# Performance work log

Measured on AMD Instinct MI355X. Metric: run time of the kernel, lower is better.

Reference implementation:

```python
import jax, jax.numpy as jnp
import numpy as np

N_ANCHORS = 9
OUTPUT_STRIDE = 16
TOP_N = 2000
NMS_IOU_THRESH = 0.7
MIN_SIZE = 0.01
EPS = 1e-7  # K.epsilon()


def setup_inputs() -> dict:
    key = jax.random.key(0)
    k1, k2 = jax.random.split(key)
    b, h, w = 8, 64, 64  # 1024px image / stride 16
    scores = jax.random.uniform(k1, (b, h, w, N_ANCHORS), jnp.float32)
    offsets = jax.random.normal(k2, (b, h, w, 4 * N_ANCHORS), jnp.float32) * 0.2
    scales = np.array([128.0, 256.0, 512.0])
    ratios = np.array([0.5, 1.0, 2.0])
    aw = (scales[:, None] * np.sqrt(ratios)[None, :]).reshape(-1)
    ah = (scales[:, None] / np.sqrt(ratios)[None, :]).reshape(-1)
    anchors = jnp.asarray(np.stack([aw, ah], axis=-1), jnp.float32)  # [9,2]
    return {"scores": scores, "offsets": offsets, "anchors": anchors}


def _pairwise_iou(a, b):
    # a: [N,4], b: [M,4] (x1,y1,x2,y2) -> [N,M]
    a = a[:, None, :]
    b = b[None, :, :]
    mins = jnp.maximum(a[..., :2], b[..., :2])
    maxs = jnp.minimum(a[..., 2:], b[..., 2:])
    wh = jnp.maximum(maxs - mins, 0.0)
    inter = wh[..., 0] * wh[..., 1]
    area_a = (a[..., 2] - a[..., 0]) * (a[..., 3] - a[..., 1])
    area_b = (b[..., 2] - b[..., 0]) * (b[..., 3] - b[..., 1])
    return inter / (area_a + area_b - inter + EPS)


def _nms_pad(boxes):
    # boxes: [N,4] already sorted by descending score (output of top_k).
    # Greedy NMS (matches tf.image.non_max_suppression semantics), keep order,
    # zero-pad suppressed tail (matches tf.pad to top_n in the original).
    N = boxes.shape[0]
    iou = _pairwise_iou(boxes, boxes)  # [N,N]
    idx = jnp.arange(N)

    def body(i, keep):
        suppress = keep[i] & (iou[i] > NMS_IOU_THRESH) & (idx > i)
        return keep & ~suppress

    keep = jax.lax.fori_loop(0, N, body, jnp.ones((N,), bool))
    sort_keys = jnp.where(keep, idx, N)          # kept indices first, in score order
    order = jnp.argsort(sort_keys)
    valid = (jnp.sort(sort_keys) < N).astype(boxes.dtype)
    return boxes[order] * valid[:, None]


def reference(scores, offsets, anchors):
    b, h, w, K = scores.shape
    off = offsets.reshape(b, h, w, K, 4)
    # anchor decode
    gx, gy = jnp.meshgrid(jnp.arange(w), jnp.arange(h))          # [h,w] each
    center = (jnp.stack([gx, gy], -1).astype(jnp.float32) + 0.5) * OUTPUT_STRIDE  # [h,w,2]
    center = center[:, :, None, :]                               # [h,w,1,2]
    img_wh = jnp.array([w, h], jnp.float32) * OUTPUT_STRIDE
    anc = anchors.reshape(1, 1, 1, K, 2)
    pred_wh = jnp.exp(off[..., 2:]) * anc / img_wh               # [b,h,w,K,2]
    pred_xcyc = (anc * off[..., :2] + center) / img_wh
    box5 = jnp.concatenate([pred_xcyc - pred_wh / 2.0,
                            pred_xcyc + pred_wh / 2.0,
                            scores[..., None]], axis=-1)         # [b,h,w,K,5]
    # filter: clip to [0,1], zero out tiny boxes
    box5 = jnp.clip(box5, 0.0, 1.0)
    wh = box5[..., 2:4] - box5[..., 0:2]
    valid = ((wh[..., 0] > MIN_SIZE) & (wh[..., 1] > MIN_SIZE)).astype(box5.dtype)
    box5 = box5 * valid[..., None]
    box5 = box5.reshape(b, -1, 5)                                # [b, h*w*K, 5]
    # per-image top-k by score, then NMS, then zero-pad to TOP_N
    _, top_i = jax.lax.top_k(box5[..., 4], TOP_N)                # [b, TOP_N]
    top_boxes = jnp.take_along_axis(box5[..., :4], top_i[..., None], axis=1)
    proposals = jax.vmap(_nms_pad)(top_boxes)                    # [b, TOP_N, 4]
    return proposals
```

## Files before the change

### kernel.cpp

```cpp
#include <hip/hip_runtime.h>
#include <stdint.h>

#pragma clang fp contract(off)

#define BATCH 8
#define HH 64
#define WW 64
#define KA 9
#define NBOX (HH * WW * KA)
#define TOPN 2000
#define NPAD 2048
#define NW 32
#define IOU_T 0.7f
#define MINSZ 0.01f
#define EPSF 1e-7f
#define TSTRIDE 33
#define CANDCAP 3072

typedef unsigned int u32;
typedef unsigned long long u64;

__device__ __forceinline__ float clamp01(float x) { return fminf(fmaxf(x, 0.0f), 1.0f); }

__device__ __forceinline__ void bar_lds()
{
    asm volatile("s_waitcnt lgkmcnt(0)" ::: "memory");
    __builtin_amdgcn_s_barrier();
}

__device__ __forceinline__ void decode_one(
    const float* __restrict__ scores, const float4* __restrict__ offsets,
    const float* __restrict__ anchors, int gid, int t,
    float4* boxOut, u32* keyOut)
{
    int k = t % KA;
    int pos = t / KA;
    int wx = pos & (WW - 1);
    int hy = pos >> 6;
    float s = scores[gid];
    float4 off = offsets[gid];
    float aw = anchors[2 * k], ah = anchors[2 * k + 1];
    float cx = ((float)wx + 0.5f) * 16.0f;
    float cy = ((float)hy + 0.5f) * 16.0f;
    float pw = (expf(off.z) * aw) / 1024.0f;
    float ph = (expf(off.w) * ah) / 1024.0f;
    float xc = (aw * off.x + cx) / 1024.0f;
    float yc = (ah * off.y + cy) / 1024.0f;
    float x1 = clamp01(xc - pw * 0.5f);
    float y1 = clamp01(yc - ph * 0.5f);
    float x2 = clamp01(xc + pw * 0.5f);
    float y2 = clamp01(yc + ph * 0.5f);
    float sc = clamp01(s);
    float m = ((x2 - x1) > MINSZ && (y2 - y1) > MINSZ) ? 1.0f : 0.0f;
    *boxOut = make_float4(x1 * m, y1 * m, x2 * m, y2 * m);
    *keyOut = __float_as_uint(sc * m);
}

__global__ __launch_bounds__(256) void decode_kernel(
    const float* __restrict__ scores, const float4* __restrict__ offsets,
    const float* __restrict__ anchors, u32* __restrict__ keys)
{
    int gid = blockIdx.x * 256 + threadIdx.x;
    int b = gid / NBOX;
    int t = gid - b * NBOX;
    float4 box; u32 key;
    decode_one(scores, offsets, anchors, gid, t, &box, &key);
    keys[gid] = key;
}

__global__ __launch_bounds__(1024) void select_kernel(
    const u32* __restrict__ keys, const float* __restrict__ scores,
    const float4* __restrict__ offsets, const float* __restrict__ anchors,
    float4* __restrict__ topBoxes)
{
    int b = blockIdx.x;
    int tid = threadIdx.x;
    const u32* kb = keys + (size_t)b * NBOX;

    __shared__ u32 hist[4096];
    __shared__ u32 suf[1024];
    __shared__ u64 sel[NPAD];
    __shared__ u64 cand[CANDCAP];
    __shared__ u32 Bsh;
    __shared__ int Rsh;
    __shared__ int ctr, cctr;

    for (int i = tid; i < 4096; i += 1024) hist[i] = 0;
    if (tid == 0) { ctr = 0; cctr = 0; }
    __syncthreads();
    for (int i = tid; i < NBOX; i += 1024)
        atomicAdd(&hist[kb[i] >> 20], 1u);
    __syncthreads();

    int r = TOPN;
    {
        u32 s = hist[4 * tid] + hist[4 * tid + 1] + hist[4 * tid + 2] + hist[4 * tid + 3];
        suf[tid] = s;
        __syncthreads();
        for (int d = 1; d < 1024; d <<= 1) {
            u32 v = (tid + d < 1024) ? suf[tid + d] : 0u;
            __syncthreads();
            suf[tid] += v;
            __syncthreads();
        }
        u32 mine = suf[tid];
        u32 nxt = (tid < 1023) ? suf[tid + 1] : 0u;
        if (mine >= (u32)r && nxt < (u32)r) {
            u32 cum = nxt;
            for (int v = 4 * tid + 3; v >= 4 * tid; --v) {
                u32 hv = hist[v];
                cum += hv;
                if (cum >= (u32)r) { Bsh = (u32)v; Rsh = r - (int)(cum - hv); break; }
            }
        }
        __syncthreads();
    }
    u32 P1 = Bsh;
    int r1 = Rsh;
    __syncthreads();

    for (int i = tid; i < NPAD; i += 1024) sel[i] = 0ull;
    __syncthreads();
    int lane = tid & 63;
    for (int i = tid; i < NBOX; i += 1024) {
        u32 key = kb[i];
        u32 top = key >> 20;
        u64 K = ((u64)key << 16) | (u64)(0xFFFFu - (u32)i);
        bool def = (top > P1);
        bool cnd = (top == P1);
        u64 bd = __ballot(def);
        u64 bc = __ballot(cnd);
        int based = 0, basec = 0;
        if (lane == 0) {
            if (bd) based = atomicAdd(&ctr, (int)__popcll(bd));
            if (bc) basec = atomicAdd(&cctr, (int)__popcll(bc));
        }
        based = __shfl(based, 0);
        basec = __shfl(basec, 0);
        if (def) {
            int slot = based + (int)__popcll(bd & ((1ull << lane) - 1ull));
            if (slot < NPAD) sel[slot] = K;
        }
        if (cnd) {
            int cslot = basec + (int)__popcll(bc & ((1ull << lane) - 1ull));
            if (cslot < CANDCAP) cand[cslot] = K;
        }
    }
    __syncthreads();
    int cc = cctr < CANDCAP ? cctr : CANDCAP;

    u64 prefix = (u64)P1;
    r = r1;
    for (int p = 0; p < 3; ++p) {
        int shift = 24 - 12 * p;
        for (int i = tid; i < 4096; i += 1024) hist[i] = 0;
        __syncthreads();
        for (int c = tid; c < cc; c += 1024) {
            u64 K = cand[c];
            if ((K >> (shift + 12)) == prefix)
                atomicAdd(&hist[(u32)((K >> shift) & 0xFFFull)], 1u);
        }
        __syncthreads();
        u32 s = hist[4 * tid] + hist[4 * tid + 1] + hist[4 * tid + 2] + hist[4 * tid + 3];
        suf[tid] = s;
        __syncthreads();
        for (int d = 1; d < 1024; d <<= 1) {
            u32 v = (tid + d < 1024) ? suf[tid + d] : 0u;
            __syncthreads();
            suf[tid] += v;
            __syncthreads();
        }
        u32 mine = suf[tid];
        u32 nxt = (tid < 1023) ? suf[tid + 1] : 0u;
        if (mine >= (u32)r && nxt < (u32)r) {
            u32 cum = nxt;
            for (int v = 4 * tid + 3; v >= 4 * tid; --v) {
                u32 hv = hist[v];
                cum += hv;
                if (cum >= (u32)r) { Bsh = (u32)v; Rsh = r - (int)(cum - hv); break; }
            }
        }
        __syncthreads();
        prefix = (prefix << 12) | (u64)Bsh;
        r = Rsh;
        __syncthreads();
    }
    u64 T48 = prefix;

    for (int c = tid; c < cc; c += 1024) {
        u64 K = cand[c];
        bool take = (K >= T48);
        u64 bal = __ballot(take);
        int base = 0;
        if (lane == 0 && bal) base = atomicAdd(&ctr, (int)__popcll(bal));
        base = __shfl(base, 0);
        if (take) {
            int slot = base + (int)__popcll(bal & ((1ull << lane) - 1ull));
            if (slot < NPAD) sel[slot] = K;
        }
    }
    __syncthreads();

    for (int k = 2; k <= NPAD; k <<= 1) {
        for (int j = k >> 1; j > 0; j >>= 1) {
#pragma unroll
            for (int n = 0; n < 2; ++n) {
                int i = tid + n * 1024;
                int ixj = i ^ j;
                if (ixj > i) {
                    bool desc = ((i & k) == 0);
                    u64 a = sel[i], c = sel[ixj];
                    if (desc ? (a < c) : (a > c)) { sel[i] = c; sel[ixj] = a; }
                }
            }
            __syncthreads();
        }
    }

    for (int i = tid; i < NPAD; i += 1024) {
        float4 v = make_float4(0, 0, 0, 0);
        if (i < TOPN) {
            u64 K = sel[i];
            int idx = 0xFFFF - (int)(K & 0xFFFFull);
            u32 kdummy;
            decode_one(scores, offsets, anchors, b * NBOX + idx, idx, &v, &kdummy);
        }
        topBoxes[b * NPAD + i] = v;
    }
}

__global__ __launch_bounds__(256) void iou_kernel(
    const float4* __restrict__ topBoxes, u64* __restrict__ sup)
{
    int gid = blockIdx.x * 256 + threadIdx.x;
    int wid = gid >> 6;
    int lane = gid & 63;
    int b = wid / TOPN;
    int r = wid - b * TOPN;

    float4 A = topBoxes[(size_t)b * NPAD + r];
    float areaA = (A.z - A.x) * (A.w - A.y);
    size_t supBase = ((size_t)b * NPAD + r) * NW;

    for (int w = r >> 6; w < NW; ++w) {
        int j = w * 64 + lane;
        float4 Bx = topBoxes[(size_t)b * NPAD + j];
        float ix1 = fmaxf(A.x, Bx.x);
        float iy1 = fmaxf(A.y, Bx.y);
        float ix2 = fminf(A.z, Bx.z);
        float iy2 = fminf(A.w, Bx.w);
        float iw = fmaxf(ix2 - ix1, 0.0f);
        float ih = fmaxf(iy2 - iy1, 0.0f);
        float inter = iw * ih;
        float areaB = (Bx.z - Bx.x) * (Bx.w - Bx.y);
        float iou = inter / (areaA + areaB - inter + EPSF);
        bool s = (iou > IOU_T) && (j > r) && (j < TOPN);
        u64 m = __ballot(s);
        if (lane == 0) sup[supBase + w] = m;
    }
}

__global__ __launch_bounds__(256) void resolve_kernel(
    const u64* __restrict__ sup, const float4* __restrict__ topBoxes,
    float4* __restrict__ out)
{
    int b = blockIdx.x;
    int tid = threadIdx.x;
    __shared__ u64 tile[2][64 * TSTRIDE];
    __shared__ u64 keep[NW];
    __shared__ u64 nzmap[NW];
    __shared__ int wbase[NW];
    if (tid < NW) keep[tid] = (tid < 31) ? ~0ull : 0xFFFFull;
    const u64* supB = sup + (size_t)b * NPAD * NW;
    unsigned* keep32 = (unsigned*)keep;

    int row = tid >> 2;
    int wcol = (tid & 3) * 8;

    {
        const uint4* src = (const uint4*)(supB + tid * 8);
        uint4 p0 = src[0], p1 = src[1], p2 = src[2], p3 = src[3];
        u64* d = &tile[0][row * TSTRIDE + wcol];
        d[0] = ((u64)p0.y << 32) | p0.x;  d[1] = ((u64)p0.w << 32) | p0.z;
        d[2] = ((u64)p1.y << 32) | p1.x;  d[3] = ((u64)p1.w << 32) | p1.z;
        d[4] = ((u64)p2.y << 32) | p2.x;  d[5] = ((u64)p2.w << 32) | p2.z;
        d[6] = ((u64)p3.y << 32) | p3.x;  d[7] = ((u64)p3.w << 32) | p3.z;
    }
    bar_lds();

    for (int w = 0; w < NW; ++w) {
        int buf = w & 1;
        uint4 n0, n1, n2, n3;
        if (w + 1 < NW) {
            const uint4* src = (const uint4*)(supB + (size_t)(w + 1) * 2048 + tid * 8);
            n0 = src[0]; n1 = src[1]; n2 = src[2]; n3 = src[3];
        }

        if (tid < 64) {
            u64 m = tile[buf][tid * TSTRIDE + w];
            u64 later = 0;
            for (int w2 = w + 1; w2 < NW; ++w2) later |= tile[buf][tid * TSTRIDE + w2];
            u64 nzAny = __ballot((m | later) != 0ull);
            u64 nzDiag = __ballot(m != 0ull);
            u32 mlo = (u32)m, mhi = (u32)(m >> 32);
            u64 kw64 = keep[w];
            u32 kwlo = (u32)__builtin_amdgcn_readfirstlane((int)(u32)kw64);
            u32 kwhi = (u32)__builtin_amdgcn_readfirstlane((int)(u32)(kw64 >> 32));
            u64 kw = ((u64)kwhi << 32) | kwlo;
            u64 rem = kw & nzDiag;
            while (rem) {
                int t2 = (int)(__ffsll((unsigned long long)rem) - 1);
                u32 alo = (u32)__builtin_amdgcn_readlane((int)mlo, t2);
                u32 ahi = (u32)__builtin_amdgcn_readlane((int)mhi, t2);
                u64 mt = ((u64)ahi << 32) | alo;
                kw &= ~mt;
                rem &= ~(mt | (1ull << t2));
            }
            if (tid == 0) { keep[w] = kw; nzmap[w] = nzAny; }
        }
        bar_lds();

        u64 gate = keep[w] & nzmap[w];
        int w2 = tid & 31;
        int grp = tid >> 5;
        if (w2 > w && gate) {
            u64 acc = 0;
#pragma unroll
            for (int q = 0; q < 8; ++q) {
                int rl = grp * 8 + q;
                if ((gate >> rl) & 1ull)
                    acc |= tile[buf][rl * TSTRIDE + w2];
            }
            if (acc) {
                u32 lo = (u32)acc, hi = (u32)(acc >> 32);
                if (lo) atomicAnd(&keep32[2 * w2], ~lo);
                if (hi) atomicAnd(&keep32[2 * w2 + 1], ~hi);
            }
        }

        if (w + 1 < NW) {
            u64* d = &tile[buf ^ 1][row * TSTRIDE + wcol];
            d[0] = ((u64)n0.y << 32) | n0.x;  d[1] = ((u64)n0.w << 32) | n0.z;
            d[2] = ((u64)n1.y << 32) | n1.x;  d[3] = ((u64)n1.w << 32) | n1.z;
            d[4] = ((u64)n2.y << 32) | n2.x;  d[5] = ((u64)n2.w << 32) | n2.z;
            d[6] = ((u64)n3.y << 32) | n3.x;  d[7] = ((u64)n3.w << 32) | n3.z;
        }
        bar_lds();
    }

    if (tid == 0) {
        int s = 0;
        for (int w2 = 0; w2 < NW; ++w2) { wbase[w2] = s; s += __popcll(keep[w2]); }
    }
    __syncthreads();
    for (int i = tid; i < TOPN; i += 256)
        out[(size_t)b * TOPN + i] = make_float4(0, 0, 0, 0);
    __syncthreads();
    for (int i = tid; i < TOPN; i += 256) {
        int wi = i >> 6, bz = i & 63;
        u64 kw = keep[wi];
        if ((kw >> bz) & 1ull) {
            int pos = wbase[wi] + __popcll(kw & ((1ull << bz) - 1ull));
            out[(size_t)b * TOPN + pos] = topBoxes[(size_t)b * NPAD + i];
        }
    }
}

extern "C" void kernel_launch(void* const* d_in, const int* in_sizes, int n_in,
                              void* d_out, int out_size, void* d_ws, size_t ws_size,
                              hipStream_t stream)
{
    const float*  scores  = (const float*)d_in[0];
    const float4* offsets = (const float4*)d_in[1];
    const float*  anchors = (const float*)d_in[2];
    float4* out = (float4*)d_out;

    char* ws = (char*)d_ws;
    u64*    sup      = (u64*)(ws);
    u32*    keys     = (u32*)(ws + 4194304);
    float4* topBoxes = (float4*)(ws + 5373952);

    decode_kernel<<<(BATCH * NBOX) / 256, 256, 0, stream>>>(scores, offsets, anchors, keys);
    select_kernel<<<BATCH, 1024, 0, stream>>>(keys, scores, offsets, anchors, topBoxes);
    iou_kernel<<<(BATCH * TOPN * 64) / 256, 256, 0, stream>>>(topBoxes, sup);
    resolve_kernel<<<BATCH, 256, 0, stream>>>(sup, topBoxes, out);
}
```

Baseline: 124.4 us.

## Build top-bits histogram in decode kernel and speed up select radix passes

Moves the first-level 12-bit key histogram out of the single-block-per-image select kernel into the massively parallel decode kernel using global atomics, with a new zero kernel to clear it. Replaces the barrier-heavy 1024-thread LDS suffix scan with a two-level single-wavefront shuffle scan for rank finding. The compaction loop now reads keys as uint4 and batches the per-wave atomic reservations over four keys. This trades an extra launch and contended global atomics for much less serial work inside the 8-block select kernel.

```diff
diff --git a/kernel.cpp b/kernel.cpp
--- a/kernel.cpp
+++ b/kernel.cpp
@@ -56,9 +56,16 @@
     *keyOut = __float_as_uint(sc * m);
 }
 
+__global__ __launch_bounds__(256) void zero_kernel(uint4* __restrict__ p, int n)
+{
+    int g = blockIdx.x * 256 + threadIdx.x;
+    if (g < n) p[g] = make_uint4(0, 0, 0, 0);
+}
+
 __global__ __launch_bounds__(256) void decode_kernel(
     const float* __restrict__ scores, const float4* __restrict__ offsets,
-    const float* __restrict__ anchors, u32* __restrict__ keys)
+    const float* __restrict__ anchors, u32* __restrict__ keys,
+    u32* __restrict__ ghist)
 {
     int gid = blockIdx.x * 256 + threadIdx.x;
     int b = gid / NBOX;
@@ -66,91 +73,126 @@
     float4 box; u32 key;
     decode_one(scores, offsets, anchors, gid, t, &box, &key);
     keys[gid] = key;
+    atomicAdd(&ghist[(b << 12) + (key >> 20)], 1u);
+}
+
+__device__ __forceinline__ void rank_find_4096(
+    const u32* __restrict__ histL, u32* __restrict__ partial,
+    int r, u32* Bsh, int* Rsh, int tid)
+{
+    partial[tid] = histL[4 * tid] + histL[4 * tid + 1]
+                 + histL[4 * tid + 2] + histL[4 * tid + 3];
+    __syncthreads();
+    if (tid < 64) {
+        int lane = tid;
+        u32 s = 0;
+#pragma unroll
+        for (int q = 0; q < 16; ++q) s += partial[lane * 16 + q];
+        u32 suf = s;
+#pragma unroll
+        for (int d = 1; d < 64; d <<= 1) {
+            u32 t = __shfl_down(suf, d);
+            if (lane + d < 64) suf += t;
+        }
+        u32 nxt = __shfl_down(suf, 1);
+        if (lane == 63) nxt = 0;
+        bool cross = (suf >= (u32)r) && (nxt < (u32)r);
+        u64 bal = __ballot(cross);
+        int L = (int)(__ffsll((unsigned long long)bal) - 1);
+        u32 above = __shfl(nxt, L);
+        u32 hv = histL[64 * L + lane];
+        u32 suf2 = hv;
+#pragma unroll
+        for (int d = 1; d < 64; d <<= 1) {
+            u32 t = __shfl_down(suf2, d);
+            if (lane + d < 64) suf2 += t;
+        }
+        u32 nxt2 = __shfl_down(suf2, 1);
+        if (lane == 63) nxt2 = 0;
+        u32 mine2 = suf2 + above;
+        nxt2 += above;
+        if (mine2 >= (u32)r && nxt2 < (u32)r) {
+            *Bsh = (u32)(64 * L + lane);
+            *Rsh = r - (int)nxt2;
+        }
+    }
+    __syncthreads();
 }
 
 __global__ __launch_bounds__(1024) void select_kernel(
-    const u32* __restrict__ keys, const float* __restrict__ scores,
-    const float4* __restrict__ offsets, const float* __restrict__ anchors,
-    float4* __restrict__ topBoxes)
+    const u32* __restrict__ keys, const u32* __restrict__ ghist,
+    const float* __restrict__ scores, const float4* __restrict__ offsets,
+    const float* __restrict__ anchors, float4* __restrict__ topBoxes)
 {
     int b = blockIdx.x;
     int tid = threadIdx.x;
+    int lane = tid & 63;
     const u32* kb = keys + (size_t)b * NBOX;
 
     __shared__ u32 hist[4096];
-    __shared__ u32 suf[1024];
+    __shared__ u32 partial[1024];
     __shared__ u64 sel[NPAD];
     __shared__ u64 cand[CANDCAP];
     __shared__ u32 Bsh;
     __shared__ int Rsh;
     __shared__ int ctr, cctr;
 
-    for (int i = tid; i < 4096; i += 1024) hist[i] = 0;
     if (tid == 0) { ctr = 0; cctr = 0; }
-    __syncthreads();
-    for (int i = tid; i < NBOX; i += 1024)
-        atomicAdd(&hist[kb[i] >> 20], 1u);
-    __syncthreads();
-
-    int r = TOPN;
-    {
-        u32 s = hist[4 * tid] + hist[4 * tid + 1] + hist[4 * tid + 2] + hist[4 * tid + 3];
-        suf[tid] = s;
-        __syncthreads();
-        for (int d = 1; d < 1024; d <<= 1) {
-            u32 v = (tid + d < 1024) ? suf[tid + d] : 0u;
-            __syncthreads();
-            suf[tid] += v;
-            __syncthreads();
-        }
-        u32 mine = suf[tid];
-        u32 nxt = (tid < 1023) ? suf[tid + 1] : 0u;
-        if (mine >= (u32)r && nxt < (u32)r) {
-            u32 cum = nxt;
-            for (int v = 4 * tid + 3; v >= 4 * tid; --v) {
-                u32 hv = hist[v];
-                cum += hv;
-                if (cum >= (u32)r) { Bsh = (u32)v; Rsh = r - (int)(cum - hv); break; }
-            }
-        }
-        __syncthreads();
-    }
+    for (int i = tid; i < 4096; i += 1024) hist[i] = ghist[(b << 12) + i];
+    for (int i = tid; i < NPAD; i += 1024) sel[i] = 0ull;
+    __syncthreads();
+    rank_find_4096(hist, partial, TOPN, &Bsh, &Rsh, tid);
     u32 P1 = Bsh;
     int r1 = Rsh;
     __syncthreads();
 
-    for (int i = tid; i < NPAD; i += 1024) sel[i] = 0ull;
-    __syncthreads();
-    int lane = tid & 63;
-    for (int i = tid; i < NBOX; i += 1024) {
-        u32 key = kb[i];
-        u32 top = key >> 20;
-        u64 K = ((u64)key << 16) | (u64)(0xFFFFu - (u32)i);
-        bool def = (top > P1);
-        bool cnd = (top == P1);
-        u64 bd = __ballot(def);
-        u64 bc = __ballot(cnd);
+    const uint4* kb4 = (const uint4*)kb;
+#pragma unroll 1
+    for (int it = 0; it < NBOX / 4096; ++it) {
+        int i4 = it * 1024 + tid;
+        uint4 kv = kb4[i4];
+        u32 karr[4] = { kv.x, kv.y, kv.z, kv.w };
+        u64 bd[4], bc[4];
+        int totd = 0, totc = 0;
+#pragma unroll
+        for (int q = 0; q < 4; ++q) {
+            u32 top = karr[q] >> 20;
+            bd[q] = __ballot(top > P1);
+            bc[q] = __ballot(top == P1);
+            totd += (int)__popcll(bd[q]);
+            totc += (int)__popcll(bc[q]);
+        }
         int based = 0, basec = 0;
         if (lane == 0) {
-            if (bd) based = atomicAdd(&ctr, (int)__popcll(bd));
-            if (bc) basec = atomicAdd(&cctr, (int)__popcll(bc));
+            if (totd) based = atomicAdd(&ctr, totd);
+            if (totc) basec = atomicAdd(&cctr, totc);
         }
         based = __shfl(based, 0);
         basec = __shfl(basec, 0);
-        if (def) {
-            int slot = based + (int)__popcll(bd & ((1ull << lane) - 1ull));
-            if (slot < NPAD) sel[slot] = K;
-        }
-        if (cnd) {
-            int cslot = basec + (int)__popcll(bc & ((1ull << lane) - 1ull));
-            if (cslot < CANDCAP) cand[cslot] = K;
+        u64 lmask = (1ull << lane) - 1ull;
+        int offd = 0, offc = 0;
+#pragma unroll
+        for (int q = 0; q < 4; ++q) {
+            u32 key = karr[q];
+            int i = i4 * 4 + q;
+            u64 K = ((u64)key << 16) | (u64)(0xFFFFu - (u32)i);
+            u32 top = key >> 20;
+            if (top > P1) {
+                int slot = based + offd + (int)__popcll(bd[q] & lmask);
+                if (slot < NPAD) sel[slot] = K;
+            } else if (top == P1) {
+                int cslot = basec + offc + (int)__popcll(bc[q] & lmask);
+                if (cslot < CANDCAP) cand[cslot] = K;
+            }
+            offd += (int)__popcll(bd[q]);
+            offc += (int)__popcll(bc[q]);
         }
     }
     __syncthreads();
     int cc = cctr < CANDCAP ? cctr : CANDCAP;
 
     u64 prefix = (u64)P1;
-    r = r1;
+    int r = r1;
     for (int p = 0; p < 3; ++p) {
         int shift = 24 - 12 * p;
         for (int i = tid; i < 4096; i += 1024) hist[i] = 0;
@@ -161,26 +203,7 @@
                 atomicAdd(&hist[(u32)((K >> shift) & 0xFFFull)], 1u);
         }
         __syncthreads();
-        u32 s = hist[4 * tid] + hist[4 * tid + 1] + hist[4 * tid + 2] + hist[4 * tid + 3];
-        suf[tid] = s;
-        __syncthreads();
-        for (int d = 1; d < 1024; d <<= 1) {
-            u32 v = (tid + d < 1024) ? suf[tid + d] : 0u;
-            __syncthreads();
-            suf[tid] += v;
-            __syncthreads();
-        }
-        u32 mine = suf[tid];
-        u32 nxt = (tid < 1023) ? suf[tid + 1] : 0u;
-        if (mine >= (u32)r && nxt < (u32)r) {
-            u32 cum = nxt;
-            for (int v = 4 * tid + 3; v >= 4 * tid; --v) {
-                u32 hv = hist[v];
-                cum += hv;
-                if (cum >= (u32)r) { Bsh = (u32)v; Rsh = r - (int)(cum - hv); break; }
-            }
-        }
-        __syncthreads();
+        rank_find_4096(hist, partial, r, &Bsh, &Rsh, tid);
         prefix = (prefix << 12) | (u64)Bsh;
         r = Rsh;
         __syncthreads();
@@ -379,9 +402,11 @@
     u64*    sup      = (u64*)(ws);
     u32*    keys     = (u32*)(ws + 4194304);
     float4* topBoxes = (float4*)(ws + 5373952);
-
-    decode_kernel<<<(BATCH * NBOX) / 256, 256, 0, stream>>>(scores, offsets, anchors, keys);
-    select_kernel<<<BATCH, 1024, 0, stream>>>(keys, scores, offsets, anchors, topBoxes);
+    u32*    ghist    = (u32*)(ws + 5636096);
+
+    zero_kernel<<<(131072 / 16 + 255) / 256, 256, 0, stream>>>((uint4*)ghist, 131072 / 16);
+    decode_kernel<<<(BATCH * NBOX) / 256, 256, 0, stream>>>(scores, offsets, anchors, keys, ghist);
+    select_kernel<<<BATCH, 1024, 0, stream>>>(keys, ghist, scores, offsets, anchors, topBoxes);
     iou_kernel<<<(BATCH * TOPN * 64) / 256, 256, 0, stream>>>(topBoxes, sup);
     resolve_kernel<<<BATCH, 256, 0, stream>>>(sup, topBoxes, out);
 }
```

New measurement: 231.5 us. 86.0% more time.
